# Optimization experiments

Measured on AMD Instinct MI355X. Metric: run time of the kernel, lower is better.

Reference implementation:

```python
import jax, jax.numpy as jnp
import numpy as np

ALPHA = 100.0   # norse SuperSpike surrogate-gradient sharpness (default)
DT = 0.001      # norse LIFBoxParameters default dt

@jax.custom_vjp
def heaviside(x):
    # spike function with SuperSpike surrogate gradient (norse method='super')
    return (x > 0).astype(x.dtype)

def _hs_fwd(x):
    return (x > 0).astype(x.dtype), x

def _hs_bwd(x, g):
    return (g / (ALPHA * jnp.abs(x) + 1.0) ** 2,)

heaviside.defvjp(_hs_fwd, _hs_bwd)


def setup_inputs() -> dict:
    key = jax.random.key(0)
    k0, k1, k2, k3, k4 = jax.random.split(key, 5)
    B, F, T = 256, 10, 8192
    inputs = jax.random.normal(k0, (B, F, T), dtype=jnp.float32)
    # learned scalar LIF parameters (one per parallel temporal layer)
    tau = jnp.array([200.0, 300.0, 600.0], dtype=jnp.float32)   # tau_mem_inv
    v_th = jnp.array([0.006, 0.008, 0.013], dtype=jnp.float32)  # thresholds
    conv_w = jax.random.normal(k1, (1, 3, 1, 1), dtype=jnp.float32) * 0.5
    conv_b = jax.random.normal(k2, (1,), dtype=jnp.float32) * 0.1
    lin_w = jax.random.normal(k3, (2, 10), dtype=jnp.float32) * 0.3
    lin_b = jax.random.normal(k4, (2,), dtype=jnp.float32) * 0.1
    return {"inputs": inputs, "tau": tau, "v_th": v_th,
            "conv_w": conv_w, "conv_b": conv_b, "lin_w": lin_w, "lin_b": lin_b}


def reference(inputs, tau, v_th, conv_w, conv_b, lin_w, lin_b):
    # inputs: [B, F, T]
    B, F, T = inputs.shape
    x_t = jnp.transpose(inputs, (2, 0, 1))          # [T, B, F], time-major
    tau3 = tau[:, None, None]                        # [3,1,1] broadcast over B,F
    vth3 = v_th[:, None, None]
    v0 = jnp.zeros((3, B, F), dtype=inputs.dtype)    # v_leak = 0 initial state

    def step(v, x):
        # LIFBox dynamics: dv = dt * tau_inv * (v_leak - v + i), v_leak=v_reset=0
        v = v + DT * tau3 * (x[None, :, :] - v)      # [3,B,F]
        z = heaviside(v - vth3)                      # spikes
        v = (1.0 - z) * v                            # reset to v_reset=0 on spike
        return v, z

    _, zs = jax.lax.scan(step, v0, x_t)              # zs: [T, 3, B, F]
    resp = jnp.transpose(zs, (2, 1, 3, 0))           # [B, 3, F, T]

    # 1x1 Conv2d over the 3 LIF channels -> [B, F, T]
    conv = jnp.einsum('bcft,c->bft', resp, conv_w[0, :, 0, 0]) + conv_b[0]
    # Linear over feature dim F=10 -> 2, output [B, 2, T]
    out = jnp.einsum('bft,of->bot', conv, lin_w) + lin_b[None, :, None]
    return out
```

## Files before the change

### kernel.cpp

```cpp
#include <hip/hip_runtime.h>


#define T_LEN 8192
#define NF 10
#define NSEQ 30
#define CHUNK 256
#define WARM 128
#define NCHUNKS 32
#define NWIN 12
#define WWIN 4
#define NROW 20
#define BUF4 (NROW * 8)

__device__ __forceinline__ float lif_step(float xx, float v, float k, float vt, bool& s) {
  float d  = __fsub_rn(xx, v);
  float p  = __fmul_rn(k, d);
  float vn = __fadd_rn(v, p);
  s = vn > vt;
  return s ? 0.0f : vn;
}

__device__ __forceinline__ float lut_sum(unsigned m, const float* lut, int o, float bias) {
  float acc = bias;
#pragma unroll
  for (int g = 0; g < 6; ++g) {
    unsigned val = (m >> (5 * g)) & 31u;
    acc += lut[(g * 2 + o) * 32 + val];
  }
  return acc;
}

#define STEP_CAP(XX, T)                                \
  {                                                    \
    bool s;                                            \
    v = lif_step((XX), v, k, vt, s);                   \
    unsigned long long ub = __ballot(s);               \
    uM = (tt == (T)) ? ub : uM;                        \
  }

__global__ __launch_bounds__(64, 4) void lif_chunked(
    const float* __restrict__ x,
    const float* __restrict__ tau,
    const float* __restrict__ vth,
    const float* __restrict__ convw,
    const float* __restrict__ convb,
    const float* __restrict__ linw,
    const float* __restrict__ linb,
    float* __restrict__ out)
{
  const int b    = blockIdx.x;
  const int cb   = blockIdx.y;
  const int lane = threadIdx.x;
  const int half = lane >> 5;
  const int j    = lane & 31;
  const bool active = j < NSEQ;
  const int c = active ? j / NF : 0;
  const int f = active ? j % NF : 0;

  __shared__ float lut[384];
  __shared__ float4 xbuf[2][BUF4];
#pragma unroll
  for (int e = 0; e < 6; ++e) {
    int id = lane + 64 * e;
    int g = id >> 6, rem = id & 63, oo = rem >> 5, val = rem & 31;
    float sacc = 0.0f;
#pragma unroll
    for (int p = 0; p < 5; ++p) {
      if (val & (1 << p)) {
        int jj = 5 * g + p;
        sacc += convw[jj / NF] * linw[oo * NF + (jj % NF)];
      }
    }
    lut[id] = sacc;
  }
  __syncthreads();

  const float k  = __fmul_rn(0.001f, tau[c]);
  const float vt = active ? vth[c] : 3.0e38f;
  const int chunk = cb * 2 + half;

  const int srow  = half * NF + f;
  const char* sbase = (const char*)&xbuf[0][0];
  const int rbyte = srow * 128 + (srow & 7) * 16;

  const int id0 = lane,        id1 = lane + 64,  id2 = (lane & 31) + 128;
  const int row0 = id0 >> 3,   row1 = id1 >> 3,  row2 = id2 >> 3;
  const int q0 = id0 & 7,      q1 = id1 & 7,     q2 = id2 & 7;
  const int ch0 = 2 * cb + row0 / NF, ch1 = 2 * cb + row1 / NF, ch2 = 2 * cb + row2 / NF;
  const int fr0 = row0 % NF,   fr1 = row1 % NF,  fr2 = row2 % NF;
  const int ts0 = (ch0 == 0) ? 0 : ch0 * CHUNK - WARM;
  const int ts1 = (ch1 == 0) ? 0 : ch1 * CHUNK - WARM;
  const int ts2 = (ch2 == 0) ? 0 : ch2 * CHUNK - WARM;
  const float4* gp0 = (const float4*)(x + ((size_t)b * NF + fr0) * (size_t)T_LEN + ts0) + q0;
  const float4* gp1 = (const float4*)(x + ((size_t)b * NF + fr1) * (size_t)T_LEN + ts1) + q1;
  const float4* gp2 = (const float4*)(x + ((size_t)b * NF + fr2) * (size_t)T_LEN + ts2) + q2;
  const int lpo0 = row0 * 8 + (q0 ^ (row0 & 7));
  const int lpo1 = row1 * 8 + (q1 ^ (row1 & 7));
  const int lpo2 = row2 * 8 + (q2 ^ (row2 & 7));
  const int adj0 = (ch0 == 0) ? -(WARM / 4) : 0;
  const int adj1 = (ch1 == 0) ? -(WARM / 4) : 0;
  const int adj2 = (ch2 == 0) ? -(WARM / 4) : 0;

  const int tt = j;
  float wsum0 = 0.0f, wsum1 = 0.0f;
#pragma unroll
  for (int f2 = 0; f2 < NF; ++f2) { wsum0 += linw[f2]; wsum1 += linw[NF + f2]; }
  const float bias0 = linb[0] + convb[0] * wsum0;
  const float bias1 = linb[1] + convb[0] * wsum1;

  const int tH = chunk * CHUNK;
  float* out0 = out + ((size_t)b * 2 + 0) * T_LEN + tH;
  float* out1 = out + ((size_t)b * 2 + 1) * T_LEN + tH;

  {
    float4 s0 = gp0[0], s1 = gp1[0], s2 = gp2[0];
    gp0 += 8; gp1 += 8; gp2 += 8;
    float4* wp = &xbuf[0][0];
    wp[lpo0] = s0; wp[lpo1] = s1; wp[lpo2] = s2;
  }

  float v = 0.0f;

#pragma unroll 1
  for (int w = 0; w < WWIN; ++w) {
    if (w + 1 == WWIN) { gp0 += adj0; gp1 += adj1; gp2 += adj2; }
    float4 rN0 = gp0[0], rN1 = gp1[0], rN2 = gp2[0];
    gp0 += 8; gp1 += 8; gp2 += 8;

    const int wb = rbyte + (w & 1) * (BUF4 * 16);
    float4 x0 = *(const float4*)(sbase + (wb ^ 0));
    float4 x1 = *(const float4*)(sbase + (wb ^ 16));
#pragma unroll
    for (int q = 0; q < 8; ++q) {
      float4 xn = x1;
      if (q + 2 < 8) xn = *(const float4*)(sbase + (wb ^ ((q + 2) << 4)));
      bool s;
      v = lif_step(x0.x, v, k, vt, s);
      v = lif_step(x0.y, v, k, vt, s);
      v = lif_step(x0.z, v, k, vt, s);
      v = lif_step(x0.w, v, k, vt, s);
      x0 = x1; x1 = xn;
    }

    float4* wp = &xbuf[(w + 1) & 1][0];
    wp[lpo0] = rN0; wp[lpo1] = rN1; wp[lpo2] = rN2;
  }
  v = (chunk == 0) ? 0.0f : v;

#pragma unroll 1
  for (int w = WWIN; w < NWIN; ++w) {
    float4 rN0, rN1, rN2;
    const bool haveNext = (w + 1 < NWIN);
    if (haveNext) {
      rN0 = gp0[0]; rN1 = gp1[0]; rN2 = gp2[0];
      gp0 += 8; gp1 += 8; gp2 += 8;
    }

    unsigned long long uM = 0;
    const int wb = rbyte + (w & 1) * (BUF4 * 16);
    float4 x0 = *(const float4*)(sbase + (wb ^ 0));
    float4 x1 = *(const float4*)(sbase + (wb ^ 16));
#pragma unroll
    for (int q = 0; q < 8; ++q) {
      float4 xn = x1;
      if (q + 2 < 8) xn = *(const float4*)(sbase + (wb ^ ((q + 2) << 4)));
      STEP_CAP(x0.x, 4 * q + 0)
      STEP_CAP(x0.y, 4 * q + 1)
      STEP_CAP(x0.z, 4 * q + 2)
      STEP_CAP(x0.w, 4 * q + 3)
      x0 = x1; x1 = xn;
    }

    const unsigned vM = half ? (unsigned)(uM >> 32) : (unsigned)uM;
    const int ow = w - WWIN;
    out0[ow * 32 + tt] = lut_sum(vM, lut, 0, bias0);
    out1[ow * 32 + tt] = lut_sum(vM, lut, 1, bias1);

    if (haveNext) {
      float4* wp = &xbuf[(w + 1) & 1][0];
      wp[lpo0] = rN0; wp[lpo1] = rN1; wp[lpo2] = rN2;
    }
  }
}

extern "C" void kernel_launch(void* const* d_in, const int* in_sizes, int n_in,
                              void* d_out, int out_size, void* d_ws, size_t ws_size,
                              hipStream_t stream) {
  const float* x     = (const float*)d_in[0];
  const float* tau   = (const float*)d_in[1];
  const float* vthp  = (const float*)d_in[2];
  const float* convw = (const float*)d_in[3];
  const float* convb = (const float*)d_in[4];
  const float* linw  = (const float*)d_in[5];
  const float* linb  = (const float*)d_in[6];
  float* out = (float*)d_out;

  const int B = in_sizes[0] / (NF * T_LEN);
  lif_chunked<<<dim3(B, NCHUNKS / 2), dim3(64), 0, stream>>>(
      x, tau, vthp, convw, convb, linw, linb, out);
}
```

Baseline: 146.5 us.

## Interleave two chunk recurrences per lane and halve the grid

Each wavefront now processes four time chunks instead of two, and each lane advances two independent LIF recurrences (chunks P and Q) interleaved step by step. Alternating the two serial chains is meant to hide the dependent-arithmetic latency and spread the fixed setup, load and ballot cost over more work. The shared staging buffer becomes a single 40-row buffer instead of a double buffer, relying on in-order LDS access within a single wave. The trade-offs are half as many blocks, more registers per lane (launch bounds lowered to 2) and less latency hiding across waves.

```diff
diff --git a/kernel.cpp b/kernel.cpp
--- a/kernel.cpp
+++ b/kernel.cpp
@@ -9,8 +9,8 @@
 #define NCHUNKS 32
 #define NWIN 12
 #define WWIN 4
-#define NROW 20
-#define BUF4 (NROW * 8)
+#define NROW 40
+#define SLOTS (NROW * 8)
 
 __device__ __forceinline__ float lif_step(float xx, float v, float k, float vt, bool& s) {
   float d  = __fsub_rn(xx, v);
@@ -30,15 +30,18 @@
   return acc;
 }
 
-#define STEP_CAP(XX, T)                                \
+#define STEP2(XP, XQ, T)                               \
   {                                                    \
-    bool s;                                            \
-    v = lif_step((XX), v, k, vt, s);                   \
-    unsigned long long ub = __ballot(s);               \
-    uM = (tt == (T)) ? ub : uM;                        \
-  }
-
-__global__ __launch_bounds__(64, 4) void lif_chunked(
+    bool sP, sQ;                                       \
+    vP = lif_step((XP), vP, k, vt, sP);                \
+    vQ = lif_step((XQ), vQ, k, vt, sQ);                \
+    unsigned long long ubP = __ballot(sP);             \
+    unsigned long long ubQ = __ballot(sQ);             \
+    uMP = (tt == (T)) ? ubP : uMP;                     \
+    uMQ = (tt == (T)) ? ubQ : uMQ;                     \
+  }
+
+__global__ __launch_bounds__(64, 2) void lif_chunked(
     const float* __restrict__ x,
     const float* __restrict__ tau,
     const float* __restrict__ vth,
@@ -58,7 +61,7 @@
   const int f = active ? j % NF : 0;
 
   __shared__ float lut[384];
-  __shared__ float4 xbuf[2][BUF4];
+  __shared__ float4 xbuf[SLOTS];
 #pragma unroll
   for (int e = 0; e < 6; ++e) {
     int id = lane + 64 * e;
@@ -77,29 +80,41 @@
 
   const float k  = __fmul_rn(0.001f, tau[c]);
   const float vt = active ? vth[c] : 3.0e38f;
-  const int chunk = cb * 2 + half;
-
-  const int srow  = half * NF + f;
-  const char* sbase = (const char*)&xbuf[0][0];
-  const int rbyte = srow * 128 + (srow & 7) * 16;
-
-  const int id0 = lane,        id1 = lane + 64,  id2 = (lane & 31) + 128;
-  const int row0 = id0 >> 3,   row1 = id1 >> 3,  row2 = id2 >> 3;
-  const int q0 = id0 & 7,      q1 = id1 & 7,     q2 = id2 & 7;
-  const int ch0 = 2 * cb + row0 / NF, ch1 = 2 * cb + row1 / NF, ch2 = 2 * cb + row2 / NF;
-  const int fr0 = row0 % NF,   fr1 = row1 % NF,  fr2 = row2 % NF;
-  const int ts0 = (ch0 == 0) ? 0 : ch0 * CHUNK - WARM;
-  const int ts1 = (ch1 == 0) ? 0 : ch1 * CHUNK - WARM;
-  const int ts2 = (ch2 == 0) ? 0 : ch2 * CHUNK - WARM;
+  const int chunkP = 4 * cb + half;
+  const int chunkQ = chunkP + 2;
+
+  const int rowP = half * NF + f;
+  const int rowQ = (2 + half) * NF + f;
+  const char* sbase  = (const char*)&xbuf[0];
+  const int rbyteP = rowP * 128 + (rowP & 7) * 16;
+  const int rbyteQ = rowQ * 128 + (rowQ & 7) * 16;
+
+  const int id0 = lane, id1 = lane + 64, id2 = lane + 128, id3 = lane + 192, id4 = lane + 256;
+  const int row0 = id0 >> 3, row1 = id1 >> 3, row2 = id2 >> 3, row3 = id3 >> 3, row4 = id4 >> 3;
+  const int q0 = id0 & 7, q1 = id1 & 7, q2 = id2 & 7, q3 = id3 & 7, q4 = id4 & 7;
+  const int chk0 = 4 * cb + row0 / NF, chk1 = 4 * cb + row1 / NF, chk2 = 4 * cb + row2 / NF,
+            chk3 = 4 * cb + row3 / NF, chk4 = 4 * cb + row4 / NF;
+  const int fr0 = row0 % NF, fr1 = row1 % NF, fr2 = row2 % NF, fr3 = row3 % NF, fr4 = row4 % NF;
+  const int ts0 = (chk0 == 0) ? 0 : chk0 * CHUNK - WARM;
+  const int ts1 = (chk1 == 0) ? 0 : chk1 * CHUNK - WARM;
+  const int ts2 = (chk2 == 0) ? 0 : chk2 * CHUNK - WARM;
+  const int ts3 = (chk3 == 0) ? 0 : chk3 * CHUNK - WARM;
+  const int ts4 = (chk4 == 0) ? 0 : chk4 * CHUNK - WARM;
   const float4* gp0 = (const float4*)(x + ((size_t)b * NF + fr0) * (size_t)T_LEN + ts0) + q0;
   const float4* gp1 = (const float4*)(x + ((size_t)b * NF + fr1) * (size_t)T_LEN + ts1) + q1;
   const float4* gp2 = (const float4*)(x + ((size_t)b * NF + fr2) * (size_t)T_LEN + ts2) + q2;
+  const float4* gp3 = (const float4*)(x + ((size_t)b * NF + fr3) * (size_t)T_LEN + ts3) + q3;
+  const float4* gp4 = (const float4*)(x + ((size_t)b * NF + fr4) * (size_t)T_LEN + ts4) + q4;
   const int lpo0 = row0 * 8 + (q0 ^ (row0 & 7));
   const int lpo1 = row1 * 8 + (q1 ^ (row1 & 7));
   const int lpo2 = row2 * 8 + (q2 ^ (row2 & 7));
-  const int adj0 = (ch0 == 0) ? -(WARM / 4) : 0;
-  const int adj1 = (ch1 == 0) ? -(WARM / 4) : 0;
-  const int adj2 = (ch2 == 0) ? -(WARM / 4) : 0;
+  const int lpo3 = row3 * 8 + (q3 ^ (row3 & 7));
+  const int lpo4 = row4 * 8 + (q4 ^ (row4 & 7));
+  const int adj0 = (chk0 == 0) ? -(WARM / 4) : 0;
+  const int adj1 = (chk1 == 0) ? -(WARM / 4) : 0;
+  const int adj2 = (chk2 == 0) ? -(WARM / 4) : 0;
+  const int adj3 = (chk3 == 0) ? -(WARM / 4) : 0;
+  const int adj4 = (chk4 == 0) ? -(WARM / 4) : 0;
 
   const int tt = j;
   float wsum0 = 0.0f, wsum1 = 0.0f;
@@ -108,77 +123,86 @@
   const float bias0 = linb[0] + convb[0] * wsum0;
   const float bias1 = linb[1] + convb[0] * wsum1;
 
-  const int tH = chunk * CHUNK;
-  float* out0 = out + ((size_t)b * 2 + 0) * T_LEN + tH;
-  float* out1 = out + ((size_t)b * 2 + 1) * T_LEN + tH;
+  float* out0 = out + ((size_t)b * 2 + 0) * T_LEN;
+  float* out1 = out + ((size_t)b * 2 + 1) * T_LEN;
+  const int tP = chunkP * CHUNK;
+  const int tQ = chunkQ * CHUNK;
 
   {
-    float4 s0 = gp0[0], s1 = gp1[0], s2 = gp2[0];
-    gp0 += 8; gp1 += 8; gp2 += 8;
-    float4* wp = &xbuf[0][0];
-    wp[lpo0] = s0; wp[lpo1] = s1; wp[lpo2] = s2;
-  }
-
-  float v = 0.0f;
+    float4 s0 = gp0[0], s1 = gp1[0], s2 = gp2[0], s3 = gp3[0], s4 = gp4[0];
+    gp0 += 8; gp1 += 8; gp2 += 8; gp3 += 8; gp4 += 8;
+    xbuf[lpo0] = s0; xbuf[lpo1] = s1; xbuf[lpo2] = s2; xbuf[lpo3] = s3; xbuf[lpo4] = s4;
+  }
+
+  float vP = 0.0f, vQ = 0.0f;
 
 #pragma unroll 1
   for (int w = 0; w < WWIN; ++w) {
-    if (w + 1 == WWIN) { gp0 += adj0; gp1 += adj1; gp2 += adj2; }
-    float4 rN0 = gp0[0], rN1 = gp1[0], rN2 = gp2[0];
-    gp0 += 8; gp1 += 8; gp2 += 8;
-
-    const int wb = rbyte + (w & 1) * (BUF4 * 16);
-    float4 x0 = *(const float4*)(sbase + (wb ^ 0));
-    float4 x1 = *(const float4*)(sbase + (wb ^ 16));
+    if (w + 1 == WWIN) { gp0 += adj0; gp1 += adj1; gp2 += adj2; gp3 += adj3; gp4 += adj4; }
+    float4 rN0 = gp0[0], rN1 = gp1[0], rN2 = gp2[0], rN3 = gp3[0], rN4 = gp4[0];
+    gp0 += 8; gp1 += 8; gp2 += 8; gp3 += 8; gp4 += 8;
+
+    float4 xP0 = *(const float4*)(sbase + (rbyteP ^ 0));
+    float4 xP1 = *(const float4*)(sbase + (rbyteP ^ 16));
+    float4 xQ0 = *(const float4*)(sbase + (rbyteQ ^ 0));
+    float4 xQ1 = *(const float4*)(sbase + (rbyteQ ^ 16));
 #pragma unroll
     for (int q = 0; q < 8; ++q) {
-      float4 xn = x1;
-      if (q + 2 < 8) xn = *(const float4*)(sbase + (wb ^ ((q + 2) << 4)));
-      bool s;
-      v = lif_step(x0.x, v, k, vt, s);
-      v = lif_step(x0.y, v, k, vt, s);
-      v = lif_step(x0.z, v, k, vt, s);
-      v = lif_step(x0.w, v, k, vt, s);
-      x0 = x1; x1 = xn;
-    }
-
-    float4* wp = &xbuf[(w + 1) & 1][0];
-    wp[lpo0] = rN0; wp[lpo1] = rN1; wp[lpo2] = rN2;
-  }
-  v = (chunk == 0) ? 0.0f : v;
+      float4 xPn = xP1, xQn = xQ1;
+      if (q + 2 < 8) {
+        xPn = *(const float4*)(sbase + (rbyteP ^ ((q + 2) << 4)));
+        xQn = *(const float4*)(sbase + (rbyteQ ^ ((q + 2) << 4)));
+      }
+      bool sP, sQ;
+      vP = lif_step(xP0.x, vP, k, vt, sP);  vQ = lif_step(xQ0.x, vQ, k, vt, sQ);
+      vP = lif_step(xP0.y, vP, k, vt, sP);  vQ = lif_step(xQ0.y, vQ, k, vt, sQ);
+      vP = lif_step(xP0.z, vP, k, vt, sP);  vQ = lif_step(xQ0.z, vQ, k, vt, sQ);
+      vP = lif_step(xP0.w, vP, k, vt, sP);  vQ = lif_step(xQ0.w, vQ, k, vt, sQ);
+      xP0 = xP1; xP1 = xPn; xQ0 = xQ1; xQ1 = xQn;
+    }
+
+    xbuf[lpo0] = rN0; xbuf[lpo1] = rN1; xbuf[lpo2] = rN2; xbuf[lpo3] = rN3; xbuf[lpo4] = rN4;
+  }
+  vP = (chunkP == 0) ? 0.0f : vP;
 
 #pragma unroll 1
   for (int w = WWIN; w < NWIN; ++w) {
-    float4 rN0, rN1, rN2;
+    float4 rN0, rN1, rN2, rN3, rN4;
     const bool haveNext = (w + 1 < NWIN);
     if (haveNext) {
-      rN0 = gp0[0]; rN1 = gp1[0]; rN2 = gp2[0];
-      gp0 += 8; gp1 += 8; gp2 += 8;
-    }
-
-    unsigned long long uM = 0;
-    const int wb = rbyte + (w & 1) * (BUF4 * 16);
-    float4 x0 = *(const float4*)(sbase + (wb ^ 0));
-    float4 x1 = *(const float4*)(sbase + (wb ^ 16));
+      rN0 = gp0[0]; rN1 = gp1[0]; rN2 = gp2[0]; rN3 = gp3[0]; rN4 = gp4[0];
+      gp0 += 8; gp1 += 8; gp2 += 8; gp3 += 8; gp4 += 8;
+    }
+
+    unsigned long long uMP = 0, uMQ = 0;
+    float4 xP0 = *(const float4*)(sbase + (rbyteP ^ 0));
+    float4 xP1 = *(const float4*)(sbase + (rbyteP ^ 16));
+    float4 xQ0 = *(const float4*)(sbase + (rbyteQ ^ 0));
+    float4 xQ1 = *(const float4*)(sbase + (rbyteQ ^ 16));
 #pragma unroll
     for (int q = 0; q < 8; ++q) {
-      float4 xn = x1;
-      if (q + 2 < 8) xn = *(const float4*)(sbase + (wb ^ ((q + 2) << 4)));
-      STEP_CAP(x0.x, 4 * q + 0)
-      STEP_CAP(x0.y, 4 * q + 1)
-      STEP_CAP(x0.z, 4 * q + 2)
-      STEP_CAP(x0.w, 4 * q + 3)
-      x0 = x1; x1 = xn;
-    }
-
-    const unsigned vM = half ? (unsigned)(uM >> 32) : (unsigned)uM;
-    const int ow = w - WWIN;
-    out0[ow * 32 + tt] = lut_sum(vM, lut, 0, bias0);
-    out1[ow * 32 + tt] = lut_sum(vM, lut, 1, bias1);
+      float4 xPn = xP1, xQn = xQ1;
+      if (q + 2 < 8) {
+        xPn = *(const float4*)(sbase + (rbyteP ^ ((q + 2) << 4)));
+        xQn = *(const float4*)(sbase + (rbyteQ ^ ((q + 2) << 4)));
+      }
+      STEP2(xP0.x, xQ0.x, 4 * q + 0)
+      STEP2(xP0.y, xQ0.y, 4 * q + 1)
+      STEP2(xP0.z, xQ0.z, 4 * q + 2)
+      STEP2(xP0.w, xQ0.w, 4 * q + 3)
+      xP0 = xP1; xP1 = xPn; xQ0 = xQ1; xQ1 = xQn;
+    }
+
+    const unsigned vMP = half ? (unsigned)(uMP >> 32) : (unsigned)uMP;
+    const unsigned vMQ = half ? (unsigned)(uMQ >> 32) : (unsigned)uMQ;
+    const int ot = (w - WWIN) * 32 + tt;
+    out0[tP + ot] = lut_sum(vMP, lut, 0, bias0);
+    out1[tP + ot] = lut_sum(vMP, lut, 1, bias1);
+    out0[tQ + ot] = lut_sum(vMQ, lut, 0, bias0);
+    out1[tQ + ot] = lut_sum(vMQ, lut, 1, bias1);
 
     if (haveNext) {
-      float4* wp = &xbuf[(w + 1) & 1][0];
-      wp[lpo0] = rN0; wp[lpo1] = rN1; wp[lpo2] = rN2;
+      xbuf[lpo0] = rN0; xbuf[lpo1] = rN1; xbuf[lpo2] = rN2; xbuf[lpo3] = rN3; xbuf[lpo4] = rN4;
     }
   }
 }
@@ -196,6 +220,6 @@
   float* out = (float*)d_out;
 
   const int B = in_sizes[0] / (NF * T_LEN);
-  lif_chunked<<<dim3(B, NCHUNKS / 2), dim3(64), 0, stream>>>(
+  lif_chunked<<<dim3(B, NCHUNKS / 4), dim3(64), 0, stream>>>(
       x, tau, vthp, convw, convb, linw, linb, out);
 }
```

Result: slower. 150.8 us (+2.9%).
